# Optimization experiments

Measured on AMD Instinct MI355X. Metric: run time of the kernel, lower is better.

## Reference

```python
import jax, jax.numpy as jnp
import numpy as np

N, C, H, W = 32, 128, 96, 96
K = 64  # num_clusters
EPS = 1e-12

def _l2norm(v, axis):
    # matches torch F.normalize: v / max(||v||, eps)
    n = jnp.sqrt(jnp.sum(v * v, axis=axis, keepdims=True))
    return v / jnp.maximum(n, EPS)

def setup_inputs() -> dict:
    key = jax.random.key(0)
    ks = jax.random.split(key, 5)
    return {
        "x": jax.random.normal(ks[0], (N, C, H, W), dtype=jnp.float32),
        "conv_w": jax.random.normal(ks[1], (K, C), dtype=jnp.float32) * 0.1,
        "centroids": jax.random.uniform(ks[2], (K, C), dtype=jnp.float32),
        "proj_w": jax.random.normal(ks[3], (C, K * C), dtype=jnp.float32) * 0.02,
        "proj_b": jax.random.normal(ks[4], (C,), dtype=jnp.float32) * 0.01,
    }

def reference(x, conv_w, centroids, proj_w, proj_b):
    n, c = x.shape[:2]
    x = _l2norm(x, axis=1)                       # normalize_input over channels
    xf = x.reshape(n, c, -1)                     # [N, C, HW]
    # 1x1 conv == per-pixel matmul: [N, K, HW]
    logits = jnp.einsum('kc,nch->nkh', conv_w, xf)
    soft = jax.nn.softmax(logits, axis=1)        # softmax over clusters
    # fused VLAD: sum_h a_{nkh} (x_{nch} - c_{kc})
    vlad = jnp.einsum('nkh,nch->nkc', soft, xf) \
         - soft.sum(axis=-1)[:, :, None] * centroids[None]
    vlad = _l2norm(vlad, axis=2)                 # intra-normalization
    vlad = vlad.reshape(n, -1)                   # [N, K*C]
    vlad = _l2norm(vlad, axis=1)
    return vlad @ proj_w.T + proj_b              # [N, C]
```

## Files before the change

kernel.cpp:

```cpp
#include <hip/hip_runtime.h>
#include <hip/hip_bf16.h>

typedef float f32x16 __attribute__((ext_vector_type(16)));
typedef short short8 __attribute__((ext_vector_type(8)));

#define N_IMG 32
#define C_CH  128
#define HW    9216
#define K_CL  64
#define EPSF  1e-12f

#define BPI   16
#define PPB   576
#define NHALF 9

#define WS_VLAD 0
#define WS_ASUM (N_IMG*K_CL*C_CH)
#define WS_ZERO (WS_ASUM + N_IMG*K_CL)
#define WS_PART WS_ZERO
#define NPART   (N_IMG*BPI)
#define WS_ASP  (WS_PART + NPART*K_CL*C_CH/2)
#define WS_STORE_TOT (WS_ASP + NPART*K_CL)

__device__ __forceinline__ unsigned short bfb(float f) {
    __hip_bfloat16 h = __float2bfloat16(f);
    return *reinterpret_cast<unsigned short*>(&h);
}
__device__ __forceinline__ float b2f(unsigned short s) {
    return __uint_as_float(((unsigned)s) << 16);
}

typedef const __attribute__((address_space(1))) void gv_t;
typedef __attribute__((address_space(3))) void lv_t;
__device__ __forceinline__ void gload16(const void* g, void* l) {
    __builtin_amdgcn_global_load_lds((gv_t*)g, (lv_t*)l, 16, 0, 0);
}
#define SBAR()  __builtin_amdgcn_s_barrier()
#define SCHED() __builtin_amdgcn_sched_barrier(0)
#define WAITL() do { asm volatile("s_waitcnt lgkmcnt(0)" ::: "memory"); SCHED(); } while (0)
#define WAITV() do { asm volatile("s_waitcnt vmcnt(0)" ::: "memory"); SCHED(); } while (0)

__global__ void k_zero(float* __restrict__ p, int cnt) {
    int i = blockIdx.x * blockDim.x + threadIdx.x;
    if (i < cnt) p[i] = 0.f;
}

__global__ __launch_bounds__(256, 2) void k_fused11(
    const float* __restrict__ x, const float* __restrict__ conv_w,
    float* __restrict__ vlad, float* __restrict__ asum,
    unsigned short* __restrict__ part, float* __restrict__ aspart, int use_part)
{
    __shared__ __align__(16) char cw_lds[64 * 256];
    __shared__ __align__(16) char xs_lds[128 * 256];
    __shared__ __align__(16) char s_lds [64 * 128];
    __shared__ __align__(16) float smpart[2][64];
    __shared__ __align__(16) float invt[64];
    __shared__ __align__(16) float sc2t[64];

    const int t  = threadIdx.x;
    const int w  = t >> 6;
    const int l  = t & 63;
    const int lp = l & 31;
    const int h  = l >> 5;
    const int n    = blockIdx.x / BPI;
    const int pblk = (blockIdx.x % BPI) * PPB;

    const int kh  = w >> 1;
    const int p   = ((w & 1) << 5) + lp;
    const int p2  = p << 1;
    const int ks  = t >> 2;
    const int st4 = t & 3;
    const float* xbase = x + (size_t)n * C_CH * HW;

    const int swzL = (lp & 7) << 4;
    const int hx   = h << 4;
    const int bCW  = (((kh << 5) + lp) << 8) | (hx ^ swzL);
    const int cB   = (w << 5) + lp;
    const int swzC = (cB & 7) << 4;
    const int bS0  = (lp << 7)        | (hx ^ swzL);
    const int bS1  = ((32 + lp) << 7) | (hx ^ swzL);
    int baseS[4];
    #pragma unroll
    for (int j = 0; j < 4; ++j)
        baseS[j] = (kh << 12) + (h << 9) + (p2 ^ (j << 4) ^ (h << 6));

    #define ISSUE_DMA(OFF) do { \
        _Pragma("unroll") \
        for (int j_ = 0; j_ < 8; ++j_) { \
            const int rloc = (l >> 4) + 4 * j_; \
            const int pxs  = ((l & 15) ^ (rloc & 7)) << 2; \
            gload16(xbase + pblk + (OFF) + (size_t)((w << 5) + rloc) * HW + pxs, \
                    xs_lds + ((((w << 5) + 4 * j_)) << 8)); \
        } } while (0)

    ISSUE_DMA(0);
    SCHED();
    #pragma unroll
    for (int r = 0; r < 16; ++r) {
        int e  = t + 256 * r;
        int k  = e >> 6;
        int c2 = (e & 63) << 1;
        unsigned pa = (unsigned)bfb(conv_w[k * C_CH + c2]) |
                      ((unsigned)bfb(conv_w[k * C_CH + c2 + 1]) << 16);
        int addr = (((k << 8) | (c2 << 1)) ^ ((k & 7) << 4));
        *reinterpret_cast<unsigned*>(cw_lds + addr) = pa;
    }

    f32x16 va0, va1;
    #pragma unroll
    for (int r = 0; r < 16; ++r) { va0[r] = 0.f; va1[r] = 0.f; }
    float asum_acc = 0.f;

    WAITL(); SBAR();

    for (int it = 0; it < NHALF; ++it) {
        if (it) { WAITL(); SBAR(); }

        const float* xp = xbase + pblk + it * 64 + p;
        float ss = 0.f;
        short8 xb[8];
        #pragma unroll
        for (int s = 0; s < 8; ++s) {
            float xv[8];
            #pragma unroll
            for (int i = 0; i < 8; ++i)
                xv[i] = xp[(size_t)(16 * s + 8 * h + i) * HW];
            #pragma unroll
            for (int i = 0; i < 8; ++i) ss += xv[i] * xv[i];
            #pragma unroll
            for (int i = 0; i < 8; ++i) xb[s][i] = (short)bfb(xv[i]);
        }
        ss += __shfl_xor(ss, 32);
        const float scn = 1.f / fmaxf(sqrtf(ss), EPSF);

        f32x16 d;
        #pragma unroll
        for (int r = 0; r < 16; ++r) d[r] = 0.f;
        #pragma unroll
        for (int s8 = 0; s8 < 8; ++s8) {
            short8 a = *reinterpret_cast<const short8*>(cw_lds + (bCW ^ (s8 << 5)));
            d = __builtin_amdgcn_mfma_f32_32x32x16_bf16(a, xb[s8], d, 0, 0, 0);
        }

        float sm = 0.f;
        #pragma unroll
        for (int r = 0; r < 16; ++r) {
            float e = __expf(d[r] * scn);
            sm += e;
            const int imm = ((r & 3) << 7) + ((r >> 2) << 10);
            *reinterpret_cast<short*>(s_lds + (baseS[r & 3] + imm)) = (short)bfb(e);
        }
        sm += __shfl_xor(sm, 32);
        if (h == 0) smpart[kh][p] = sm;
        WAITL(); SBAR();

        const float inv = 1.f / (smpart[0][p] + smpart[1][p]);
        if (kh == 0 && h == 0) { invt[p] = inv; sc2t[p] = scn * inv; }
        WAITL(); SBAR();

        WAITV();

        #pragma unroll
        for (int sp = 0; sp < 4; ++sp) {
            const int boffp = (sp << 6) + (h << 5);
            const int a0 = (cB << 8) + (boffp ^ swzC);
            float4 f0 = *reinterpret_cast<const float4*>(xs_lds + a0);
            float4 f1 = *reinterpret_cast<const float4*>(xs_lds + (a0 ^ 16));
            const int pix0 = (sp << 4) + (h << 3);
            float4 s2a = *reinterpret_cast<const float4*>(sc2t + pix0);
            float4 s2b = *reinterpret_cast<const float4*>(sc2t + pix0 + 4);
            short8 bf;
            bf[0] = (short)bfb(f0.x * s2a.x); bf[1] = (short)bfb(f0.y * s2a.y);
            bf[2] = (short)bfb(f0.z * s2a.z); bf[3] = (short)bfb(f0.w * s2a.w);
            bf[4] = (short)bfb(f1.x * s2b.x); bf[5] = (short)bfb(f1.y * s2b.y);
            bf[6] = (short)bfb(f1.z * s2b.z); bf[7] = (short)bfb(f1.w * s2b.w);
            short8 s0 = *reinterpret_cast<const short8*>(s_lds + (bS0 ^ (sp << 5)));
            short8 s1 = *reinterpret_cast<const short8*>(s_lds + (bS1 ^ (sp << 5)));
            va0 = __builtin_amdgcn_mfma_f32_32x32x16_bf16(s0, bf, va0, 0, 0, 0);
            va1 = __builtin_amdgcn_mfma_f32_32x32x16_bf16(s1, bf, va1, 0, 0, 0);
        }

        WAITL();
        if (it + 1 < NHALF) ISSUE_DMA((it + 1) * 64);
        SCHED();

        {
            const int rowb = ks << 7;
            const int swz  = (ks & 7) << 4;
            const float* ivp = invt + (st4 << 4);
            float a = 0.f;
            #pragma unroll
            for (int g = 0; g < 2; ++g) {
                int off = (st4 << 5) | (g << 4);
                short8 u = *reinterpret_cast<const short8*>(s_lds + (rowb | (off ^ swz)));
                float4 ia = *reinterpret_cast<const float4*>(ivp + g * 8);
                float4 ib = *reinterpret_cast<const float4*>(ivp + g * 8 + 4);
                a += b2f((unsigned short)u[0]) * ia.x + b2f((unsigned short)u[1]) * ia.y +
                     b2f((unsigned short)u[2]) * ia.z + b2f((unsigned short)u[3]) * ia.w;
                a += b2f((unsigned short)u[4]) * ib.x + b2f((unsigned short)u[5]) * ib.y +
                     b2f((unsigned short)u[6]) * ib.z + b2f((unsigned short)u[7]) * ib.w;
            }
            asum_acc += a;
        }
    }

    if (use_part) {
        unsigned short* pb_ = part + (size_t)blockIdx.x * (K_CL * C_CH) + cB;
        #pragma unroll
        for (int r = 0; r < 16; ++r) {
            const int kr = (r & 3) + 8 * (r >> 2) + 4 * h;
            pb_[(kr)      * C_CH] = bfb(va0[r]);
            pb_[(32 + kr) * C_CH] = bfb(va1[r]);
        }
        float vv = asum_acc;
        vv += __shfl_xor(vv, 1);
        vv += __shfl_xor(vv, 2);
        if (st4 == 0) aspart[blockIdx.x * K_CL + ks] = vv;
    } else {
        float* vb = vlad + (size_t)n * K_CL * C_CH;
        #pragma unroll
        for (int r = 0; r < 16; ++r) {
            const int kr = (r & 3) + 8 * (r >> 2) + 4 * h;
            atomicAdd(vb + (kr)      * C_CH + cB, va0[r]);
            atomicAdd(vb + (32 + kr) * C_CH + cB, va1[r]);
        }
        float vv = asum_acc;
        vv += __shfl_xor(vv, 1);
        vv += __shfl_xor(vv, 2);
        if (st4 == 0) atomicAdd(asum + n * K_CL + ks, vv);
    }
    #undef ISSUE_DMA
}

__global__ void k_rows_part(float* __restrict__ vlad, const unsigned short* __restrict__ part,
                            const float* __restrict__ aspart,
                            const float* __restrict__ cent)
{
    const int bx = blockIdx.x;
    const int n = bx >> 6, k = bx & 63;
    const int c = threadIdx.x;
    const int b0 = n * BPI;
    float v = 0.f, a = 0.f;
    #pragma unroll
    for (int b = 0; b < BPI; ++b) {
        v += b2f(part[(size_t)(b0 + b) * (K_CL * C_CH) + k * C_CH + c]);
        a += aspart[(b0 + b) * K_CL + k];
    }
    v -= a * cent[k * C_CH + c];
    float ssq = v * v;
    #pragma unroll
    for (int m = 32; m >= 1; m >>= 1) ssq += __shfl_xor(ssq, m);
    __shared__ float sb[2];
    if ((threadIdx.x & 63) == 0) sb[threadIdx.x >> 6] = ssq;
    __syncthreads();
    float tot = sb[0] + sb[1];
    float sc = 1.f / fmaxf(sqrtf(tot), EPSF);
    vlad[((size_t)n * K_CL + k) * C_CH + c] = v * sc;
}

__global__ void k_rows(float* __restrict__ vlad, const float* __restrict__ asum,
                       const float* __restrict__ cent)
{
    const int bx = blockIdx.x;
    const int n = bx >> 6, k = bx & 63;
    const int c = threadIdx.x;
    float a = asum[n * K_CL + k];
    size_t idx = ((size_t)n * K_CL + k) * C_CH + c;
    float v = vlad[idx] - a * cent[k * C_CH + c];
    float ssq = v * v;
    #pragma unroll
    for (int m = 32; m >= 1; m >>= 1) ssq += __shfl_xor(ssq, m);
    __shared__ float sb[2];
    if ((threadIdx.x & 63) == 0) sb[threadIdx.x >> 6] = ssq;
    __syncthreads();
    float tot = sb[0] + sb[1];
    float sc = 1.f / fmaxf(sqrtf(tot), EPSF);
    vlad[idx] = v * sc;
}

__global__ __launch_bounds__(256) void k_proj3(
    const float* __restrict__ vlad, const float* __restrict__ pw,
    const float* __restrict__ pbias, float* __restrict__ out)
{
    const int j  = blockIdx.x;
    const int n0 = blockIdx.y << 2;
    const int t  = threadIdx.x;
    const float4* wp = (const float4*)(pw + (size_t)j * (K_CL * C_CH));
    float4 wr[8];
    #pragma unroll
    for (int r = 0; r < 8; ++r) wr[r] = wp[t + 256 * r];
    __shared__ float sb[4], sb2[4];
    const float bias = pbias[j];
    #pragma unroll
    for (int u = 0; u < 4; ++u) {
        const int n = n0 + u;
        const float4* vp = (const float4*)(vlad + (size_t)n * (K_CL * C_CH));
        float s = 0.f, nn = 0.f;
        #pragma unroll
        for (int r = 0; r < 8; ++r) {
            float4 a = vp[t + 256 * r];
            s  += a.x * wr[r].x + a.y * wr[r].y + a.z * wr[r].z + a.w * wr[r].w;
            nn += a.x * a.x + a.y * a.y + a.z * a.z + a.w * a.w;
        }
        #pragma unroll
        for (int m = 32; m >= 1; m >>= 1) {
            s  += __shfl_xor(s, m);
            nn += __shfl_xor(nn, m);
        }
        if ((t & 63) == 0) { sb[t >> 6] = s; sb2[t >> 6] = nn; }
        __syncthreads();
        if (t == 0) {
            float tot = sb[0] + sb[1] + sb[2] + sb[3];
            float tss = sb2[0] + sb2[1] + sb2[2] + sb2[3];
            float inv = 1.f / fmaxf(sqrtf(tss), EPSF);
            out[n * C_CH + j] = tot * inv + bias;
        }
        __syncthreads();
    }
}

extern "C" void kernel_launch(void* const* d_in, const int* in_sizes, int n_in,
                              void* d_out, int out_size, void* d_ws, size_t ws_size,
                              hipStream_t stream)
{
    const float* x      = (const float*)d_in[0];
    const float* conv_w = (const float*)d_in[1];
    const float* cent   = (const float*)d_in[2];
    const float* pw     = (const float*)d_in[3];
    const float* pbias  = (const float*)d_in[4];
    float* out = (float*)d_out;
    float* ws  = (float*)d_ws;

    float* vlad            = ws + WS_VLAD;
    float* asum            = ws + WS_ASUM;
    unsigned short* part   = (unsigned short*)(ws + WS_PART);
    float* aspart          = ws + WS_ASP;

    const int use_part = (ws_size >= (size_t)WS_STORE_TOT * sizeof(float)) ? 1 : 0;

    if (!use_part) {
        hipLaunchKernelGGL(k_zero, dim3((WS_ZERO + 255) / 256), dim3(256), 0, stream,
                           ws, WS_ZERO);
    }
    hipLaunchKernelGGL(k_fused11, dim3(N_IMG * BPI), dim3(256), 0, stream,
                       x, conv_w, vlad, asum, part, aspart, use_part);
    if (use_part) {
        hipLaunchKernelGGL(k_rows_part, dim3(N_IMG * K_CL), dim3(C_CH), 0, stream,
                           vlad, part, aspart, cent);
    } else {
        hipLaunchKernelGGL(k_rows, dim3(N_IMG * K_CL), dim3(C_CH), 0, stream,
                           vlad, asum, cent);
    }
    hipLaunchKernelGGL(k_proj3, dim3(C_CH, N_IMG / 4), dim3(256), 0, stream,
                       vlad, pw, pbias, out);
}
```

Baseline: 61.20 us.

## Split fused kernel into producer and consumer warp groups with double-buffered LDS

The fused kernel now runs 512 threads as two groups. The producer half loads x from global memory, computes per-pixel norms, and writes the normalized bf16 tiles into double-buffered LDS in two layouts. The consumer half runs the logit MFMA, softmax, and VLAD accumulation, so it no longer reloads x twice (once from global, once through the DMA) or rescales per pixel. This is meant to overlap global-load latency with MFMA work and to remove the duplicate read of x. In exchange it adds block barriers, uses more LDS, and drops to one block per CU, and it also normalizes x to bf16 before the second GEMM, which changes rounding.

```diff
diff --git a/kernel.cpp b/kernel.cpp
--- a/kernel.cpp
+++ b/kernel.cpp
@@ -12,7 +12,7 @@
 
 #define BPI   16
 #define PPB   576
-#define NHALF 9
+#define NTILE 9
 
 #define WS_VLAD 0
 #define WS_ASUM (N_IMG*K_CL*C_CH)
@@ -30,11 +30,6 @@
     return __uint_as_float(((unsigned)s) << 16);
 }
 
-typedef const __attribute__((address_space(1))) void gv_t;
-typedef __attribute__((address_space(3))) void lv_t;
-__device__ __forceinline__ void gload16(const void* g, void* l) {
-    __builtin_amdgcn_global_load_lds((gv_t*)g, (lv_t*)l, 16, 0, 0);
-}
 #define SBAR()  __builtin_amdgcn_s_barrier()
 #define SCHED() __builtin_amdgcn_sched_barrier(0)
 #define WAITL() do { asm volatile("s_waitcnt lgkmcnt(0)" ::: "memory"); SCHED(); } while (0)
@@ -45,146 +40,181 @@
     if (i < cnt) p[i] = 0.f;
 }
 
-__global__ __launch_bounds__(256, 2) void k_fused11(
+__global__ __launch_bounds__(512, 1) void k_fusedPC(
     const float* __restrict__ x, const float* __restrict__ conv_w,
     float* __restrict__ vlad, float* __restrict__ asum,
     unsigned short* __restrict__ part, float* __restrict__ aspart, int use_part)
 {
     __shared__ __align__(16) char cw_lds[64 * 256];
-    __shared__ __align__(16) char xs_lds[128 * 256];
-    __shared__ __align__(16) char s_lds [64 * 128];
+    __shared__ __align__(16) char xpc[2][64 * 256];
+    __shared__ __align__(16) char xcp[2][128 * 128];
+    __shared__ __align__(16) char s_lds[64 * 128];
     __shared__ __align__(16) float smpart[2][64];
+    __shared__ __align__(16) float sspart[2][64];
     __shared__ __align__(16) float invt[64];
-    __shared__ __align__(16) float sc2t[64];
 
     const int t  = threadIdx.x;
+    const int n    = blockIdx.x / BPI;
+    const int pblk = (blockIdx.x % BPI) * PPB;
+    const float* xbase = x + (size_t)n * C_CH * HW;
+    const bool isC = (t < 256);
+
     const int w  = t >> 6;
     const int l  = t & 63;
     const int lp = l & 31;
     const int h  = l >> 5;
-    const int n    = blockIdx.x / BPI;
-    const int pblk = (blockIdx.x % BPI) * PPB;
-
-    const int kh  = w >> 1;
-    const int p   = ((w & 1) << 5) + lp;
-    const int p2  = p << 1;
-    const int ks  = t >> 2;
-    const int st4 = t & 3;
-    const float* xbase = x + (size_t)n * C_CH * HW;
-
+    const int kh = w >> 1;
+    const int p  = ((w & 1) << 5) + lp;
+    const int p2 = p << 1;
+    const int ks = t >> 2, st4 = t & 3;
     const int swzL = (lp & 7) << 4;
     const int hx   = h << 4;
     const int bCW  = (((kh << 5) + lp) << 8) | (hx ^ swzL);
+    const int bPC  = (p << 8) | (hx ^ ((p & 7) << 4));
     const int cB   = (w << 5) + lp;
-    const int swzC = (cB & 7) << 4;
-    const int bS0  = (lp << 7)        | (hx ^ swzL);
+    const int bXf  = (cB << 7) | (hx ^ ((cB & 7) << 4));
+    const int bS0  = (lp << 7) | (hx ^ swzL);
     const int bS1  = ((32 + lp) << 7) | (hx ^ swzL);
     int baseS[4];
     #pragma unroll
     for (int j = 0; j < 4; ++j)
         baseS[j] = (kh << 12) + (h << 9) + (p2 ^ (j << 4) ^ (h << 6));
 
-    #define ISSUE_DMA(OFF) do { \
-        _Pragma("unroll") \
-        for (int j_ = 0; j_ < 8; ++j_) { \
-            const int rloc = (l >> 4) + 4 * j_; \
-            const int pxs  = ((l & 15) ^ (rloc & 7)) << 2; \
-            gload16(xbase + pblk + (OFF) + (size_t)((w << 5) + rloc) * HW + pxs, \
-                    xs_lds + ((((w << 5) + 4 * j_)) << 8)); \
-        } } while (0)
-
-    ISSUE_DMA(0);
-    SCHED();
-    #pragma unroll
-    for (int r = 0; r < 16; ++r) {
-        int e  = t + 256 * r;
-        int k  = e >> 6;
-        int c2 = (e & 63) << 1;
-        unsigned pa = (unsigned)bfb(conv_w[k * C_CH + c2]) |
-                      ((unsigned)bfb(conv_w[k * C_CH + c2 + 1]) << 16);
-        int addr = (((k << 8) | (c2 << 1)) ^ ((k & 7) << 4));
-        *reinterpret_cast<unsigned*>(cw_lds + addr) = pa;
-    }
+    const int tp   = t & 255;
+    const int wp   = tp >> 6;
+    const int lP   = tp & 63;
+    const int lpP  = lP & 31;
+    const int hP   = lP >> 5;
+    const int pxP  = ((wp & 1) << 5) + lpP;
+    const int s0P  = (wp >> 1) << 2;
+    const int pairI = wp >> 1;
+    const int bWpc  = pxP << 8;
+    const int swzPC = (pxP & 7) << 4;
 
     f32x16 va0, va1;
     #pragma unroll
     for (int r = 0; r < 16; ++r) { va0[r] = 0.f; va1[r] = 0.f; }
     float asum_acc = 0.f;
-
-    WAITL(); SBAR();
-
-    for (int it = 0; it < NHALF; ++it) {
-        if (it) { WAITL(); SBAR(); }
-
-        const float* xp = xbase + pblk + it * 64 + p;
-        float ss = 0.f;
-        short8 xb[8];
-        #pragma unroll
-        for (int s = 0; s < 8; ++s) {
-            float xv[8];
-            #pragma unroll
-            for (int i = 0; i < 8; ++i)
-                xv[i] = xp[(size_t)(16 * s + 8 * h + i) * HW];
-            #pragma unroll
-            for (int i = 0; i < 8; ++i) ss += xv[i] * xv[i];
-            #pragma unroll
-            for (int i = 0; i < 8; ++i) xb[s][i] = (short)bfb(xv[i]);
-        }
-        ss += __shfl_xor(ss, 32);
-        const float scn = 1.f / fmaxf(sqrtf(ss), EPSF);
-
-        f32x16 d;
-        #pragma unroll
-        for (int r = 0; r < 16; ++r) d[r] = 0.f;
-        #pragma unroll
-        for (int s8 = 0; s8 < 8; ++s8) {
-            short8 a = *reinterpret_cast<const short8*>(cw_lds + (bCW ^ (s8 << 5)));
-            d = __builtin_amdgcn_mfma_f32_32x32x16_bf16(a, xb[s8], d, 0, 0, 0);
-        }
-
-        float sm = 0.f;
+    float xv[4][8];
+
+    #define P_LOAD(TL) do { \
+        const float* xp_ = xbase + pblk + (TL) * 64 + pxP; \
+        _Pragma("unroll") \
+        for (int si = 0; si < 4; ++si) \
+            _Pragma("unroll") \
+            for (int i = 0; i < 8; ++i) \
+                xv[si][i] = xp_[(size_t)(16 * (s0P + si) + 8 * hP + i) * HW]; \
+    } while (0)
+
+    #define P_SSQ() do { \
+        float ss_ = 0.f; \
+        _Pragma("unroll") \
+        for (int si = 0; si < 4; ++si) \
+            _Pragma("unroll") \
+            for (int i = 0; i < 8; ++i) ss_ += xv[si][i] * xv[si][i]; \
+        ss_ += __shfl_xor(ss_, 32); \
+        if (hP == 0) sspart[pairI][pxP] = ss_; \
+    } while (0)
+
+    #define P_WRITE(XPCB, XCPB) do { \
+        const float scn_ = 1.f / fmaxf(sqrtf(sspart[0][pxP] + sspart[1][pxP]), EPSF); \
+        _Pragma("unroll") \
+        for (int si = 0; si < 4; ++si) { \
+            short8 xn_; \
+            _Pragma("unroll") \
+            for (int i = 0; i < 8; ++i) xn_[i] = (short)bfb(xv[si][i] * scn_); \
+            const int m_ = ((s0P + si) << 1) + hP; \
+            *reinterpret_cast<short8*>((XPCB) + (bWpc | ((m_ << 4) ^ swzPC))) = xn_; \
+            _Pragma("unroll") \
+            for (int i = 0; i < 8; ++i) { \
+                const int c_ = 16 * (s0P + si) + 8 * hP + i; \
+                *reinterpret_cast<short*>((XCPB) + ((c_ << 7) | ((pxP << 1) ^ (i << 4)))) = (short)xn_[i]; \
+            } \
+        } \
+    } while (0)
+
+    if (!isC) {
+        P_LOAD(0);
+    } else {
         #pragma unroll
         for (int r = 0; r < 16; ++r) {
-            float e = __expf(d[r] * scn);
-            sm += e;
-            const int imm = ((r & 3) << 7) + ((r >> 2) << 10);
-            *reinterpret_cast<short*>(s_lds + (baseS[r & 3] + imm)) = (short)bfb(e);
-        }
-        sm += __shfl_xor(sm, 32);
-        if (h == 0) smpart[kh][p] = sm;
+            int e  = t + 256 * r;
+            int k  = e >> 6;
+            int c2 = (e & 63) << 1;
+            unsigned pa = (unsigned)bfb(conv_w[k * C_CH + c2]) |
+                          ((unsigned)bfb(conv_w[k * C_CH + c2 + 1]) << 16);
+            int addr = (((k << 8) | (c2 << 1)) ^ ((k & 7) << 4));
+            *reinterpret_cast<unsigned*>(cw_lds + addr) = pa;
+        }
+    }
+    WAITL(); SBAR();
+    if (!isC) { WAITV(); P_SSQ(); }
+    WAITL(); SBAR();
+    if (!isC) { P_WRITE(xpc[0], xcp[0]); P_LOAD(1); }
+    WAITL(); SBAR();
+
+    for (int it = 0; it < NTILE; ++it) {
+        char* xpcB = xpc[it & 1];
+        char* xcpB = xcp[it & 1];
+        char* xpcN = xpc[(it + 1) & 1];
+        char* xcpN = xcp[(it + 1) & 1];
+
+        if (isC) {
+            f32x16 d;
+            #pragma unroll
+            for (int r = 0; r < 16; ++r) d[r] = 0.f;
+            #pragma unroll
+            for (int s = 0; s < 8; ++s) {
+                short8 a = *reinterpret_cast<const short8*>(cw_lds + (bCW ^ (s << 5)));
+                short8 b = *reinterpret_cast<const short8*>(xpcB + (bPC ^ (s << 5)));
+                d = __builtin_amdgcn_mfma_f32_32x32x16_bf16(a, b, d, 0, 0, 0);
+            }
+            float sm = 0.f;
+            #pragma unroll
+            for (int r = 0; r < 16; ++r) {
+                float e = __expf(d[r]);
+                sm += e;
+                const int imm = ((r & 3) << 7) + ((r >> 2) << 10);
+                *reinterpret_cast<short*>(s_lds + (baseS[r & 3] + imm)) = (short)bfb(e);
+            }
+            sm += __shfl_xor(sm, 32);
+            if (h == 0) smpart[kh][p] = sm;
+        } else if (it + 1 < NTILE) {
+            WAITV();
+            P_SSQ();
+        }
         WAITL(); SBAR();
 
-        const float inv = 1.f / (smpart[0][p] + smpart[1][p]);
-        if (kh == 0 && h == 0) { invt[p] = inv; sc2t[p] = scn * inv; }
+        if (isC) {
+            if (kh == 0 && h == 0)
+                invt[p] = 1.f / (smpart[0][p] + smpart[1][p]);
+        } else if (it + 1 < NTILE) {
+            P_WRITE(xpcN, xcpN);
+            if (it + 2 < NTILE) P_LOAD(it + 2);
+        }
         WAITL(); SBAR();
 
-        WAITV();
-
-        #pragma unroll
-        for (int sp = 0; sp < 4; ++sp) {
-            const int boffp = (sp << 6) + (h << 5);
-            const int a0 = (cB << 8) + (boffp ^ swzC);
-            float4 f0 = *reinterpret_cast<const float4*>(xs_lds + a0);
-            float4 f1 = *reinterpret_cast<const float4*>(xs_lds + (a0 ^ 16));
-            const int pix0 = (sp << 4) + (h << 3);
-            float4 s2a = *reinterpret_cast<const float4*>(sc2t + pix0);
-            float4 s2b = *reinterpret_cast<const float4*>(sc2t + pix0 + 4);
-            short8 bf;
-            bf[0] = (short)bfb(f0.x * s2a.x); bf[1] = (short)bfb(f0.y * s2a.y);
-            bf[2] = (short)bfb(f0.z * s2a.z); bf[3] = (short)bfb(f0.w * s2a.w);
-            bf[4] = (short)bfb(f1.x * s2b.x); bf[5] = (short)bfb(f1.y * s2b.y);
-            bf[6] = (short)bfb(f1.z * s2b.z); bf[7] = (short)bfb(f1.w * s2b.w);
-            short8 s0 = *reinterpret_cast<const short8*>(s_lds + (bS0 ^ (sp << 5)));
-            short8 s1 = *reinterpret_cast<const short8*>(s_lds + (bS1 ^ (sp << 5)));
-            va0 = __builtin_amdgcn_mfma_f32_32x32x16_bf16(s0, bf, va0, 0, 0, 0);
-            va1 = __builtin_amdgcn_mfma_f32_32x32x16_bf16(s1, bf, va1, 0, 0, 0);
-        }
-
-        WAITL();
-        if (it + 1 < NHALF) ISSUE_DMA((it + 1) * 64);
-        SCHED();
-
-        {
+        if (isC) {
+            #pragma unroll
+            for (int sp = 0; sp < 4; ++sp) {
+                short8 xr = *reinterpret_cast<const short8*>(xcpB + (bXf ^ (sp << 5)));
+                const int pix0 = (sp << 4) + (h << 3);
+                float4 ia = *reinterpret_cast<const float4*>(invt + pix0);
+                float4 ib = *reinterpret_cast<const float4*>(invt + pix0 + 4);
+                short8 bf;
+                bf[0] = (short)bfb(b2f((unsigned short)xr[0]) * ia.x);
+                bf[1] = (short)bfb(b2f((unsigned short)xr[1]) * ia.y);
+                bf[2] = (short)bfb(b2f((unsigned short)xr[2]) * ia.z);
+                bf[3] = (short)bfb(b2f((unsigned short)xr[3]) * ia.w);
+                bf[4] = (short)bfb(b2f((unsigned short)xr[4]) * ib.x);
+                bf[5] = (short)bfb(b2f((unsigned short)xr[5]) * ib.y);
+                bf[6] = (short)bfb(b2f((unsigned short)xr[6]) * ib.z);
+                bf[7] = (short)bfb(b2f((unsigned short)xr[7]) * ib.w);
+                short8 sA = *reinterpret_cast<const short8*>(s_lds + (bS0 ^ (sp << 5)));
+                short8 sB = *reinterpret_cast<const short8*>(s_lds + (bS1 ^ (sp << 5)));
+                va0 = __builtin_amdgcn_mfma_f32_32x32x16_bf16(sA, bf, va0, 0, 0, 0);
+                va1 = __builtin_amdgcn_mfma_f32_32x32x16_bf16(sB, bf, va1, 0, 0, 0);
+            }
             const int rowb = ks << 7;
             const int swz  = (ks & 7) << 4;
             const float* ivp = invt + (st4 << 4);
@@ -193,43 +223,48 @@
             for (int g = 0; g < 2; ++g) {
                 int off = (st4 << 5) | (g << 4);
                 short8 u = *reinterpret_cast<const short8*>(s_lds + (rowb | (off ^ swz)));
-                float4 ia = *reinterpret_cast<const float4*>(ivp + g * 8);
-                float4 ib = *reinterpret_cast<const float4*>(ivp + g * 8 + 4);
-                a += b2f((unsigned short)u[0]) * ia.x + b2f((unsigned short)u[1]) * ia.y +
-                     b2f((unsigned short)u[2]) * ia.z + b2f((unsigned short)u[3]) * ia.w;
-                a += b2f((unsigned short)u[4]) * ib.x + b2f((unsigned short)u[5]) * ib.y +
-                     b2f((unsigned short)u[6]) * ib.z + b2f((unsigned short)u[7]) * ib.w;
+                float4 na = *reinterpret_cast<const float4*>(ivp + g * 8);
+                float4 nb = *reinterpret_cast<const float4*>(ivp + g * 8 + 4);
+                a += b2f((unsigned short)u[0]) * na.x + b2f((unsigned short)u[1]) * na.y +
+                     b2f((unsigned short)u[2]) * na.z + b2f((unsigned short)u[3]) * na.w;
+                a += b2f((unsigned short)u[4]) * nb.x + b2f((unsigned short)u[5]) * nb.y +
+                     b2f((unsigned short)u[6]) * nb.z + b2f((unsigned short)u[7]) * nb.w;
             }
             asum_acc += a;
         }
-    }
-
-    if (use_part) {
-        unsigned short* pb_ = part + (size_t)blockIdx.x * (K_CL * C_CH) + cB;
-        #pragma unroll
-        for (int r = 0; r < 16; ++r) {
-            const int kr = (r & 3) + 8 * (r >> 2) + 4 * h;
-            pb_[(kr)      * C_CH] = bfb(va0[r]);
-            pb_[(32 + kr) * C_CH] = bfb(va1[r]);
-        }
-        float vv = asum_acc;
-        vv += __shfl_xor(vv, 1);
-        vv += __shfl_xor(vv, 2);
-        if (st4 == 0) aspart[blockIdx.x * K_CL + ks] = vv;
-    } else {
-        float* vb = vlad + (size_t)n * K_CL * C_CH;
-        #pragma unroll
-        for (int r = 0; r < 16; ++r) {
-            const int kr = (r & 3) + 8 * (r >> 2) + 4 * h;
-            atomicAdd(vb + (kr)      * C_CH + cB, va0[r]);
-            atomicAdd(vb + (32 + kr) * C_CH + cB, va1[r]);
-        }
-        float vv = asum_acc;
-        vv += __shfl_xor(vv, 1);
-        vv += __shfl_xor(vv, 2);
-        if (st4 == 0) atomicAdd(asum + n * K_CL + ks, vv);
-    }
-    #undef ISSUE_DMA
+        SBAR();
+    }
+
+    if (isC) {
+        if (use_part) {
+            unsigned short* pb_ = part + (size_t)blockIdx.x * (K_CL * C_CH) + cB;
+            #pragma unroll
+            for (int r = 0; r < 16; ++r) {
+                const int kr = (r & 3) + 8 * (r >> 2) + 4 * h;
+                pb_[(kr)      * C_CH] = bfb(va0[r]);
+                pb_[(32 + kr) * C_CH] = bfb(va1[r]);
+            }
+            float vv = asum_acc;
+            vv += __shfl_xor(vv, 1);
+            vv += __shfl_xor(vv, 2);
+            if (st4 == 0) aspart[blockIdx.x * K_CL + ks] = vv;
+        } else {
+            float* vb = vlad + (size_t)n * K_CL * C_CH;
+            #pragma unroll
+            for (int r = 0; r < 16; ++r) {
+                const int kr = (r & 3) + 8 * (r >> 2) + 4 * h;
+                atomicAdd(vb + (kr)      * C_CH + cB, va0[r]);
+                atomicAdd(vb + (32 + kr) * C_CH + cB, va1[r]);
+            }
+            float vv = asum_acc;
+            vv += __shfl_xor(vv, 1);
+            vv += __shfl_xor(vv, 2);
+            if (st4 == 0) atomicAdd(asum + n * K_CL + ks, vv);
+        }
+    }
+    #undef P_LOAD
+    #undef P_SSQ
+    #undef P_WRITE
 }
 
 __global__ void k_rows_part(float* __restrict__ vlad, const unsigned short* __restrict__ part,
@@ -342,7 +377,7 @@
         hipLaunchKernelGGL(k_zero, dim3((WS_ZERO + 255) / 256), dim3(256), 0, stream,
                            ws, WS_ZERO);
     }
-    hipLaunchKernelGGL(k_fused11, dim3(N_IMG * BPI), dim3(256), 0, stream,
+    hipLaunchKernelGGL(k_fusedPC, dim3(N_IMG * BPI), dim3(512), 0, stream,
                        x, conv_w, vlad, asum, part, aspart, use_part);
     if (use_part) {
         hipLaunchKernelGGL(k_rows_part, dim3(N_IMG * K_CL), dim3(C_CH), 0, stream,
```

Result: slower. 69.87 us (+14.2%).
